# Performance work log

Hardware: AMD Instinct MI355X
Metric: run time of the kernel (lower is better)

## Reference

```python
import jax, jax.numpy as jnp
import numpy as np

N = 100000
E = 1600000
DIMS = [64, 64, 64, 32]  # input -> hidden -> hidden -> num_classes
NEG_SLOPE = 0.01  # F.leaky_relu default


def setup_inputs() -> dict:
    key = jax.random.key(0)
    ks = jax.random.split(key, 8)
    inp = {
        "x": jax.random.normal(ks[0], (N, DIMS[0]), dtype=jnp.float32),
        "edge_index": jax.random.randint(ks[1], (2, E), 0, N, dtype=jnp.int64),
    }
    # GCNConv linear weights (glorot-ish scale) and biases
    for i in range(3):
        d_in, d_out = DIMS[i], DIMS[i + 1]
        scale = (2.0 / (d_in + d_out)) ** 0.5
        inp[f"W{i+1}"] = jax.random.normal(ks[2 + i], (d_in, d_out), dtype=jnp.float32) * scale
        inp[f"b{i+1}"] = jnp.zeros((d_out,), dtype=jnp.float32)
    return inp


def _gcn_conv(x, src, dst, norm, W, b):
    # x' = D^-1/2 (A+I) D^-1/2 (x W) + b
    h = x @ W                                   # [N, d_out]
    msg = h[src] * norm[:, None]                # gather + edge scaling  [E+N, d_out]
    out = jax.ops.segment_sum(msg, dst, num_segments=N)  # scatter-add
    return out + b


def reference(x, edge_index, W1, b1, W2, b2, W3, b3):
    loops = jnp.arange(N, dtype=edge_index.dtype)
    src = jnp.concatenate([edge_index[0], loops])  # add self-loops
    dst = jnp.concatenate([edge_index[1], loops])
    deg = jax.ops.segment_sum(jnp.ones_like(src, dtype=x.dtype), dst, num_segments=N)
    deg_isqrt = jax.lax.rsqrt(deg)              # deg >= 1 due to self-loops
    norm = deg_isqrt[src] * deg_isqrt[dst]      # [E+N]

    embeddings = []
    h = x
    for i, (W, b) in enumerate([(W1, b1), (W2, b2), (W3, b3)]):
        h = _gcn_conv(h, src, dst, norm, W, b)
        if i < 2:
            h = jnp.where(h >= 0, h, NEG_SLOPE * h)  # leaky_relu
        embeddings.append(h)
    return tuple(embeddings)
```

## Files before the change

kernel.cpp:

```cpp
#include <hip/hip_runtime.h>
#include <hip/hip_bf16.h>

typedef __hip_bfloat16 bf16;
typedef __attribute__((ext_vector_type(8))) short bf16x8;
typedef __attribute__((ext_vector_type(4))) short bf16x4;
typedef __attribute__((ext_vector_type(4))) float f32x4;

constexpr int BLK = 256;
constexpr int SCAN2_T = 512;
constexpr int NBLK = 400;

__device__ inline float s2f(short s) {
    union { unsigned u; float f; } z;
    z.u = ((unsigned)(unsigned short)s) << 16;
    return z.f;
}
__device__ inline short f2s(float f) {
    union { bf16 h; short s; } u;
    u.h = __float2bfloat16(f);
    return u.s;
}

__global__ void bucket_hist(const int* __restrict__ dst, int* __restrict__ blockhist,
                            int E, int EPB, int NB) {
    __shared__ int h[512];
    for (int i = threadIdx.x; i < NB; i += BLK) h[i] = 0;
    __syncthreads();
    int lo = blockIdx.x * EPB;
    int hi = min(E, lo + EPB);
    for (int t = lo + threadIdx.x; t < hi; t += BLK)
        atomicAdd(&h[dst[t] >> 8], 1);
    __syncthreads();
    for (int i = threadIdx.x; i < NB; i += BLK)
        blockhist[i * NBLK + blockIdx.x] = h[i];
}

__global__ void colscan_kernel(int* __restrict__ blockhist, int* __restrict__ btotal) {
    __shared__ int s[SCAN2_T];
    int b = blockIdx.x;
    int t = threadIdx.x;
    int v = (t < NBLK) ? blockhist[b * NBLK + t] : 0;
    s[t] = v;
    __syncthreads();
    for (int off = 1; off < SCAN2_T; off <<= 1) {
        int add = (t >= off) ? s[t - off] : 0;
        __syncthreads();
        s[t] += add;
        __syncthreads();
    }
    if (t < NBLK) blockhist[b * NBLK + t] = s[t] - v;
    if (t == SCAN2_T - 1) btotal[b] = s[SCAN2_T - 1];
}

__global__ void scan2_kernel(int* __restrict__ bsum, int nb) {
    __shared__ int s[SCAN2_T];
    int t = threadIdx.x;
    int v = (t < nb) ? bsum[t] : 0;
    s[t] = v;
    __syncthreads();
    for (int off = 1; off < SCAN2_T; off <<= 1) {
        int add = (t >= off) ? s[t - off] : 0;
        __syncthreads();
        s[t] += add;
        __syncthreads();
    }
    if (t < nb) bsum[t] = s[t] - v;
}

__global__ void bucket_scatter(const int* __restrict__ src, const int* __restrict__ dst,
                               const int* __restrict__ blockhist, const int* __restrict__ bbase,
                               int2* __restrict__ ssd, int E, int EPB, int NB) {
    __shared__ int h[512];
    for (int i = threadIdx.x; i < NB; i += BLK)
        h[i] = bbase[i] + blockhist[i * NBLK + blockIdx.x];
    __syncthreads();
    int lo = blockIdx.x * EPB;
    int hi = min(E, lo + EPB);
    for (int t = lo + threadIdx.x; t < hi; t += BLK) {
        int d = dst[t];
        int pos = atomicAdd(&h[d >> 8], 1);
        int2 e; e.x = src[t]; e.y = d;
        ssd[pos] = e;
    }
}

__global__ void bucket_csr(const int2* __restrict__ ssd, const int* __restrict__ bbase,
                           int* __restrict__ col, int* __restrict__ deg,
                           int* __restrict__ row_ptr, float* __restrict__ dinv,
                           int N, int E, int NB) {
    __shared__ int dloc[256];
    __shared__ int ss[256];
    __shared__ int cur[256];
    int b = blockIdx.x;
    int t = threadIdx.x;
    int lo = bbase[b];
    int hi = (b + 1 < NB) ? bbase[b + 1] : E;
    dloc[t] = 0;
    __syncthreads();
    for (int j = lo + t; j < hi; j += BLK)
        atomicAdd(&dloc[ssd[j].y & 255], 1);
    __syncthreads();
    int own = dloc[t];
    ss[t] = own;
    __syncthreads();
    for (int off = 1; off < 256; off <<= 1) {
        int add = (t >= off) ? ss[t - off] : 0;
        __syncthreads();
        ss[t] += add;
        __syncthreads();
    }
    int excl = ss[t] - own;
    cur[t] = lo + excl;
    int node = (b << 8) + t;
    if (node < N) {
        deg[node] = own;
        row_ptr[node] = lo + excl;
        dinv[node] = rsqrtf((float)own + 1.0f);
    }
    __syncthreads();
    for (int j = lo + t; j < hi; j += BLK) {
        int2 e = ssd[j];
        int p = atomicAdd(&cur[e.y & 255], 1);
        col[p] = e.x;
    }
}

__global__ void wconv_all(const float* __restrict__ W1, const float* __restrict__ W2,
                          const float* __restrict__ W3, bf16* __restrict__ WT1,
                          bf16* __restrict__ WT2, bf16* __restrict__ WT3) {
    int idx = blockIdx.x * blockDim.x + threadIdx.x;
    if (idx < 4096) {
        int k = idx >> 6, c = idx & 63;
        WT1[c * 64 + k] = __float2bfloat16(W1[idx]);
    } else if (idx < 8192) {
        int i = idx - 4096, k = i >> 6, c = i & 63;
        WT2[c * 64 + k] = __float2bfloat16(W2[i]);
    } else if (idx < 10240) {
        int i = idx - 8192, k = i >> 5, c = i & 31;
        WT3[c * 64 + k] = __float2bfloat16(W3[i]);
    }
}

template <int DOUT, bool AF32>
__global__ void mfma_gemm(const void* __restrict__ inv, const bf16* __restrict__ WT,
                          const float* __restrict__ dinv, bf16* __restrict__ hlin, int n) {
    constexpr int NT = DOUT / 16;
    const int lane = threadIdx.x & 63;
    const int wave = threadIdx.x >> 6;
    const int q = lane >> 4;
    const int l16 = lane & 15;
    const int row0 = blockIdx.x * 64 + wave * 16;

    int arow = row0 + l16;
    if (arow >= n) arow = n - 1;

    bf16x8 a0, a1;
    if (AF32) {
        const float* in = (const float*)inv;
        const float* p = in + (size_t)arow * 64 + q * 8;
        float4 f0 = *(const float4*)(p);
        float4 f1 = *(const float4*)(p + 4);
        float4 g0 = *(const float4*)(p + 32);
        float4 g1 = *(const float4*)(p + 36);
        bf16 t0[8] = {__float2bfloat16(f0.x), __float2bfloat16(f0.y), __float2bfloat16(f0.z), __float2bfloat16(f0.w),
                      __float2bfloat16(f1.x), __float2bfloat16(f1.y), __float2bfloat16(f1.z), __float2bfloat16(f1.w)};
        bf16 t1[8] = {__float2bfloat16(g0.x), __float2bfloat16(g0.y), __float2bfloat16(g0.z), __float2bfloat16(g0.w),
                      __float2bfloat16(g1.x), __float2bfloat16(g1.y), __float2bfloat16(g1.z), __float2bfloat16(g1.w)};
        __builtin_memcpy(&a0, t0, 16);
        __builtin_memcpy(&a1, t1, 16);
    } else {
        const bf16* in = (const bf16*)inv;
        a0 = *(const bf16x8*)(in + (size_t)arow * 64 + q * 8);
        a1 = *(const bf16x8*)(in + (size_t)arow * 64 + 32 + q * 8);
    }

    f32x4 acc[NT];
#pragma unroll
    for (int ct = 0; ct < NT; ++ct) {
        const bf16* wrow = WT + (size_t)(ct * 16 + l16) * 64 + q * 8;
        bf16x8 b0 = *(const bf16x8*)(wrow);
        bf16x8 b1 = *(const bf16x8*)(wrow + 32);
        f32x4 c = {0.f, 0.f, 0.f, 0.f};
        c = __builtin_amdgcn_mfma_f32_16x16x32_bf16(a0, b0, c, 0, 0, 0);
        c = __builtin_amdgcn_mfma_f32_16x16x32_bf16(a1, b1, c, 0, 0, 0);
        acc[ct] = c;
    }

    float dv[4];
#pragma unroll
    for (int r = 0; r < 4; ++r) {
        int rr = row0 + q * 4 + r;
        dv[r] = (rr < n) ? dinv[rr] : 0.0f;
    }
#pragma unroll
    for (int ct = 0; ct < NT; ++ct) {
#pragma unroll
        for (int r = 0; r < 4; ++r) {
            int rr = row0 + q * 4 + r;
            if (rr < n)
                hlin[(size_t)rr * DOUT + ct * 16 + l16] = __float2bfloat16(acc[ct][r] * dv[r]);
        }
    }
}

template <bool LEAKY>
__global__ void agg64_kernel(const int* __restrict__ row_ptr, const int* __restrict__ deg,
                             const int* __restrict__ col, const bf16* __restrict__ hlin,
                             const float* __restrict__ dinv, const float* __restrict__ b,
                             float* __restrict__ out, bf16* __restrict__ actb, int n) {
    int node = (blockIdx.x * blockDim.x + threadIdx.x) >> 6;
    int lane = threadIdx.x & 63;
    if (node >= n) return;
    const int g = lane >> 3;
    const int fl = lane & 7;

    float acc[8] = {0.f, 0.f, 0.f, 0.f, 0.f, 0.f, 0.f, 0.f};
    if (g == 0) {
        bf16x8 sv = *(const bf16x8*)(hlin + (size_t)node * 64 + (fl << 3));
#pragma unroll
        for (int k = 0; k < 8; ++k) acc[k] = s2f(sv[k]);
    }

    const int beg = row_ptr[node];
    const int end = beg + deg[node];
    int j = beg;
    for (; j + 16 <= end; j += 16) {
        int c0 = col[j + g];
        int c1 = col[j + 8 + g];
        bf16x8 v0 = *(const bf16x8*)(hlin + (size_t)c0 * 64 + (fl << 3));
        bf16x8 v1 = *(const bf16x8*)(hlin + (size_t)c1 * 64 + (fl << 3));
#pragma unroll
        for (int k = 0; k < 8; ++k) acc[k] += s2f(v0[k]) + s2f(v1[k]);
    }
    if (j + 8 <= end) {
        int c = col[j + g];
        bf16x8 v = *(const bf16x8*)(hlin + (size_t)c * 64 + (fl << 3));
#pragma unroll
        for (int k = 0; k < 8; ++k) acc[k] += s2f(v[k]);
        j += 8;
    }
    if (j + g < end) {
        int c = col[j + g];
        bf16x8 v = *(const bf16x8*)(hlin + (size_t)c * 64 + (fl << 3));
#pragma unroll
        for (int k = 0; k < 8; ++k) acc[k] += s2f(v[k]);
    }

#pragma unroll
    for (int k = 0; k < 8; ++k) acc[k] += __shfl_xor(acc[k], 8);
#pragma unroll
    for (int k = 0; k < 8; ++k) acc[k] += __shfl_xor(acc[k], 16);
#pragma unroll
    for (int k = 0; k < 8; ++k) acc[k] += __shfl_xor(acc[k], 32);

    const float dv = dinv[node];
    const float4 bb0 = *(const float4*)(b + (fl << 3));
    const float4 bb1 = *(const float4*)(b + (fl << 3) + 4);
    float vals[8];
    vals[0] = acc[0] * dv + bb0.x;
    vals[1] = acc[1] * dv + bb0.y;
    vals[2] = acc[2] * dv + bb0.z;
    vals[3] = acc[3] * dv + bb0.w;
    vals[4] = acc[4] * dv + bb1.x;
    vals[5] = acc[5] * dv + bb1.y;
    vals[6] = acc[6] * dv + bb1.z;
    vals[7] = acc[7] * dv + bb1.w;
    if (LEAKY) {
#pragma unroll
        for (int k = 0; k < 8; ++k) vals[k] = (vals[k] >= 0.0f) ? vals[k] : 0.01f * vals[k];
    }
    if (g == 0) {
        float* op = out + (size_t)node * 64 + (fl << 3);
        f32x4 o0 = {vals[0], vals[1], vals[2], vals[3]};
        f32x4 o1 = {vals[4], vals[5], vals[6], vals[7]};
        __builtin_nontemporal_store(o0, (f32x4*)op);
        __builtin_nontemporal_store(o1, (f32x4*)(op + 4));
        if (actb) {
            bf16x8 ob;
#pragma unroll
            for (int k = 0; k < 8; ++k) ob[k] = f2s(vals[k]);
            *(bf16x8*)(actb + (size_t)node * 64 + (fl << 3)) = ob;
        }
    }
}

__global__ void agg32_kernel(const int* __restrict__ row_ptr, const int* __restrict__ deg,
                             const int* __restrict__ col, const bf16* __restrict__ hlin,
                             const float* __restrict__ dinv, const float* __restrict__ b,
                             float* __restrict__ out, int n) {
    int node = (blockIdx.x * blockDim.x + threadIdx.x) >> 6;
    int lane = threadIdx.x & 63;
    if (node >= n) return;
    const int g = lane >> 3;
    const int fl = lane & 7;

    float acc[4] = {0.f, 0.f, 0.f, 0.f};
    if (g == 0) {
        bf16x4 sv = *(const bf16x4*)(hlin + (size_t)node * 32 + (fl << 2));
#pragma unroll
        for (int k = 0; k < 4; ++k) acc[k] = s2f(sv[k]);
    }

    const int beg = row_ptr[node];
    const int end = beg + deg[node];
    int j = beg;
    for (; j + 16 <= end; j += 16) {
        int c0 = col[j + g];
        int c1 = col[j + 8 + g];
        bf16x4 v0 = *(const bf16x4*)(hlin + (size_t)c0 * 32 + (fl << 2));
        bf16x4 v1 = *(const bf16x4*)(hlin + (size_t)c1 * 32 + (fl << 2));
#pragma unroll
        for (int k = 0; k < 4; ++k) acc[k] += s2f(v0[k]) + s2f(v1[k]);
    }
    if (j + 8 <= end) {
        int c = col[j + g];
        bf16x4 v = *(const bf16x4*)(hlin + (size_t)c * 32 + (fl << 2));
#pragma unroll
        for (int k = 0; k < 4; ++k) acc[k] += s2f(v[k]);
        j += 8;
    }
    if (j + g < end) {
        int c = col[j + g];
        bf16x4 v = *(const bf16x4*)(hlin + (size_t)c * 32 + (fl << 2));
#pragma unroll
        for (int k = 0; k < 4; ++k) acc[k] += s2f(v[k]);
    }

#pragma unroll
    for (int k = 0; k < 4; ++k) acc[k] += __shfl_xor(acc[k], 8);
#pragma unroll
    for (int k = 0; k < 4; ++k) acc[k] += __shfl_xor(acc[k], 16);
#pragma unroll
    for (int k = 0; k < 4; ++k) acc[k] += __shfl_xor(acc[k], 32);

    const float dv = dinv[node];
    const float4 bb = *(const float4*)(b + (fl << 2));
    float vals[4];
    vals[0] = acc[0] * dv + bb.x;
    vals[1] = acc[1] * dv + bb.y;
    vals[2] = acc[2] * dv + bb.z;
    vals[3] = acc[3] * dv + bb.w;
    if (g == 0) {
        f32x4 o = {vals[0], vals[1], vals[2], vals[3]};
        __builtin_nontemporal_store(o, (f32x4*)(out + (size_t)node * 32 + (fl << 2)));
    }
}

extern "C" void kernel_launch(void* const* d_in, const int* in_sizes, int n_in,
                              void* d_out, int out_size, void* d_ws, size_t ws_size,
                              hipStream_t stream) {
    const float* x  = (const float*)d_in[0];
    const int*   ei = (const int*)d_in[1];
    const float* W1 = (const float*)d_in[2];
    const float* b1 = (const float*)d_in[3];
    const float* W2 = (const float*)d_in[4];
    const float* b2 = (const float*)d_in[5];
    const float* W3 = (const float*)d_in[6];
    const float* b3 = (const float*)d_in[7];
    float* out = (float*)d_out;

    const int N = in_sizes[0] / 64;
    const int E = in_sizes[1] / 2;
    const int* src = ei;
    const int* dst = ei + E;

    const int NB  = (N + 255) >> 8;
    const int EPB = (E + NBLK - 1) / NBLK;

    char* w = (char*)d_ws;
    auto take = [&](size_t bytes) { char* p = w; w += (bytes + 15) & ~(size_t)15; return p; };
    int*   col       = (int*)take((size_t)E * 4);
    int2*  ssd       = (int2*)take((size_t)E * 8);
    bf16*  hlin      = (bf16*)take((size_t)N * 64 * 2);
    bf16*  actb      = (bf16*)take((size_t)N * 64 * 2);
    bf16*  WT1       = (bf16*)take(64 * 64 * 2);
    bf16*  WT2       = (bf16*)take(64 * 64 * 2);
    bf16*  WT3       = (bf16*)take(32 * 64 * 2);
    int*   deg       = (int*)take((size_t)N * 4);
    int*   row_ptr   = (int*)take((size_t)N * 4);
    float* dinv      = (float*)take((size_t)N * 4);
    int*   blockhist = (int*)take((size_t)NB * NBLK * 4);
    int*   btotal    = (int*)take((size_t)SCAN2_T * 4);

    float* out0 = out;
    float* out1 = out + (size_t)N * 64;
    float* out2 = out + (size_t)N * 128;

    const int gemmBlocks = (N + 63) / 64;

    bucket_hist<<<NBLK, BLK, 0, stream>>>(dst, blockhist, E, EPB, NB);
    colscan_kernel<<<NB, SCAN2_T, 0, stream>>>(blockhist, btotal);
    scan2_kernel<<<1, SCAN2_T, 0, stream>>>(btotal, NB);
    bucket_scatter<<<NBLK, BLK, 0, stream>>>(src, dst, blockhist, btotal, ssd, E, EPB, NB);
    bucket_csr<<<NB, BLK, 0, stream>>>(ssd, btotal, col, deg, row_ptr, dinv, N, E, NB);

    wconv_all<<<40, BLK, 0, stream>>>(W1, W2, W3, WT1, WT2, WT3);

    mfma_gemm<64, true><<<gemmBlocks, BLK, 0, stream>>>(x, WT1, dinv, hlin, N);
    agg64_kernel<true><<<((size_t)N * 64 + BLK - 1) / BLK, BLK, 0, stream>>>(
        row_ptr, deg, col, hlin, dinv, b1, out0, actb, N);

    mfma_gemm<64, false><<<gemmBlocks, BLK, 0, stream>>>(actb, WT2, dinv, hlin, N);
    agg64_kernel<true><<<((size_t)N * 64 + BLK - 1) / BLK, BLK, 0, stream>>>(
        row_ptr, deg, col, hlin, dinv, b2, out1, actb, N);

    mfma_gemm<32, false><<<gemmBlocks, BLK, 0, stream>>>(actb, WT3, dinv, hlin, N);
    agg32_kernel<<<((size_t)N * 64 + BLK - 1) / BLK, BLK, 0, stream>>>(
        row_ptr, deg, col, hlin, dinv, b3, out2, N);
}
```

Measured before the change: 314.9 us.

## Pack four nodes per wavefront in aggregation kernels with padded zero row

Aggregation kernels now assign four nodes to each 64-lane wavefront, 16 lanes per node, with two neighbor slots instead of eight. The neighbor loop runs a uniform trip count (max degree among the four nodes), sends out-of-range lanes to a zeroed pad row in hlin, and prefetches the next column index. This cuts the wasted lanes that occur when a node with about 16 neighbors is spread over eight slots, and it removes two shuffle-reduction stages. The cost is a longer serial chain per node and divergence padding toward the largest degree in each group. For agg32 the pad index 2*n points at the same zeroed row under 32-wide addressing, which relies on the extra padded allocation.

```diff
diff --git a/kernel.cpp b/kernel.cpp
--- a/kernel.cpp
+++ b/kernel.cpp
@@ -208,52 +208,48 @@
                              const int* __restrict__ col, const bf16* __restrict__ hlin,
                              const float* __restrict__ dinv, const float* __restrict__ b,
                              float* __restrict__ out, bf16* __restrict__ actb, int n) {
-    int node = (blockIdx.x * blockDim.x + threadIdx.x) >> 6;
-    int lane = threadIdx.x & 63;
-    if (node >= n) return;
-    const int g = lane >> 3;
+    const int wid = (blockIdx.x * blockDim.x + threadIdx.x) >> 6;
+    const int lane = threadIdx.x & 63;
+    const int sub = lane >> 4;
+    const int g = (lane >> 3) & 1;
     const int fl = lane & 7;
-
-    float acc[8] = {0.f, 0.f, 0.f, 0.f, 0.f, 0.f, 0.f, 0.f};
-    if (g == 0) {
-        bf16x8 sv = *(const bf16x8*)(hlin + (size_t)node * 64 + (fl << 3));
+    const int node = wid * 4 + sub;
+    const int PAD = n;
+
+    const bool valid = node < n;
+    const int nc = valid ? node : n - 1;
+    const int beg = row_ptr[nc];
+    const int dg = valid ? deg[nc] : 0;
+    const int end = beg + dg;
+
+    float acc[8];
+    {
+        int c0 = (valid && g == 0) ? node : PAD;
+        bf16x8 sv = *(const bf16x8*)(hlin + (size_t)c0 * 64 + (fl << 3));
 #pragma unroll
         for (int k = 0; k < 8; ++k) acc[k] = s2f(sv[k]);
     }
 
-    const int beg = row_ptr[node];
-    const int end = beg + deg[node];
-    int j = beg;
-    for (; j + 16 <= end; j += 16) {
-        int c0 = col[j + g];
-        int c1 = col[j + 8 + g];
-        bf16x8 v0 = *(const bf16x8*)(hlin + (size_t)c0 * 64 + (fl << 3));
-        bf16x8 v1 = *(const bf16x8*)(hlin + (size_t)c1 * 64 + (fl << 3));
-#pragma unroll
-        for (int k = 0; k < 8; ++k) acc[k] += s2f(v0[k]) + s2f(v1[k]);
-    }
-    if (j + 8 <= end) {
-        int c = col[j + g];
+    int m = dg;
+    m = max(m, __shfl_xor(m, 16));
+    m = max(m, __shfl_xor(m, 32));
+    const int iters = (m + 1) >> 1;
+
+    int idx = beg + g;
+    int cv = col[idx < end ? idx : 0];
+    for (int j = 0; j < iters; ++j) {
+        const int c = (idx < end) ? cv : PAD;
+        idx += 2;
+        cv = col[idx < end ? idx : 0];
         bf16x8 v = *(const bf16x8*)(hlin + (size_t)c * 64 + (fl << 3));
 #pragma unroll
         for (int k = 0; k < 8; ++k) acc[k] += s2f(v[k]);
-        j += 8;
-    }
-    if (j + g < end) {
-        int c = col[j + g];
-        bf16x8 v = *(const bf16x8*)(hlin + (size_t)c * 64 + (fl << 3));
-#pragma unroll
-        for (int k = 0; k < 8; ++k) acc[k] += s2f(v[k]);
     }
 
 #pragma unroll
     for (int k = 0; k < 8; ++k) acc[k] += __shfl_xor(acc[k], 8);
-#pragma unroll
-    for (int k = 0; k < 8; ++k) acc[k] += __shfl_xor(acc[k], 16);
-#pragma unroll
-    for (int k = 0; k < 8; ++k) acc[k] += __shfl_xor(acc[k], 32);
-
-    const float dv = dinv[node];
+
+    const float dv = dinv[nc];
     const float4 bb0 = *(const float4*)(b + (fl << 3));
     const float4 bb1 = *(const float4*)(b + (fl << 3) + 4);
     float vals[8];
@@ -269,7 +265,7 @@
 #pragma unroll
         for (int k = 0; k < 8; ++k) vals[k] = (vals[k] >= 0.0f) ? vals[k] : 0.01f * vals[k];
     }
-    if (g == 0) {
+    if (valid && g == 0) {
         float* op = out + (size_t)node * 64 + (fl << 3);
         f32x4 o0 = {vals[0], vals[1], vals[2], vals[3]};
         f32x4 o1 = {vals[4], vals[5], vals[6], vals[7]};
@@ -288,59 +284,55 @@
                              const int* __restrict__ col, const bf16* __restrict__ hlin,
                              const float* __restrict__ dinv, const float* __restrict__ b,
                              float* __restrict__ out, int n) {
-    int node = (blockIdx.x * blockDim.x + threadIdx.x) >> 6;
-    int lane = threadIdx.x & 63;
-    if (node >= n) return;
-    const int g = lane >> 3;
+    const int wid = (blockIdx.x * blockDim.x + threadIdx.x) >> 6;
+    const int lane = threadIdx.x & 63;
+    const int sub = lane >> 4;
+    const int g = (lane >> 3) & 1;
     const int fl = lane & 7;
-
-    float acc[4] = {0.f, 0.f, 0.f, 0.f};
-    if (g == 0) {
-        bf16x4 sv = *(const bf16x4*)(hlin + (size_t)node * 32 + (fl << 2));
+    const int node = wid * 4 + sub;
+    const int PAD = 2 * n;
+
+    const bool valid = node < n;
+    const int nc = valid ? node : n - 1;
+    const int beg = row_ptr[nc];
+    const int dg = valid ? deg[nc] : 0;
+    const int end = beg + dg;
+
+    float acc[4];
+    {
+        int c0 = (valid && g == 0) ? node : PAD;
+        bf16x4 sv = *(const bf16x4*)(hlin + (size_t)c0 * 32 + (fl << 2));
 #pragma unroll
         for (int k = 0; k < 4; ++k) acc[k] = s2f(sv[k]);
     }
 
-    const int beg = row_ptr[node];
-    const int end = beg + deg[node];
-    int j = beg;
-    for (; j + 16 <= end; j += 16) {
-        int c0 = col[j + g];
-        int c1 = col[j + 8 + g];
-        bf16x4 v0 = *(const bf16x4*)(hlin + (size_t)c0 * 32 + (fl << 2));
-        bf16x4 v1 = *(const bf16x4*)(hlin + (size_t)c1 * 32 + (fl << 2));
-#pragma unroll
-        for (int k = 0; k < 4; ++k) acc[k] += s2f(v0[k]) + s2f(v1[k]);
-    }
-    if (j + 8 <= end) {
-        int c = col[j + g];
+    int m = dg;
+    m = max(m, __shfl_xor(m, 16));
+    m = max(m, __shfl_xor(m, 32));
+    const int iters = (m + 1) >> 1;
+
+    int idx = beg + g;
+    int cv = col[idx < end ? idx : 0];
+    for (int j = 0; j < iters; ++j) {
+        const int c = (idx < end) ? cv : PAD;
+        idx += 2;
+        cv = col[idx < end ? idx : 0];
         bf16x4 v = *(const bf16x4*)(hlin + (size_t)c * 32 + (fl << 2));
 #pragma unroll
         for (int k = 0; k < 4; ++k) acc[k] += s2f(v[k]);
-        j += 8;
-    }
-    if (j + g < end) {
-        int c = col[j + g];
-        bf16x4 v = *(const bf16x4*)(hlin + (size_t)c * 32 + (fl << 2));
-#pragma unroll
-        for (int k = 0; k < 4; ++k) acc[k] += s2f(v[k]);
     }
 
 #pragma unroll
     for (int k = 0; k < 4; ++k) acc[k] += __shfl_xor(acc[k], 8);
-#pragma unroll
-    for (int k = 0; k < 4; ++k) acc[k] += __shfl_xor(acc[k], 16);
-#pragma unroll
-    for (int k = 0; k < 4; ++k) acc[k] += __shfl_xor(acc[k], 32);
-
-    const float dv = dinv[node];
+
+    const float dv = dinv[nc];
     const float4 bb = *(const float4*)(b + (fl << 2));
     float vals[4];
     vals[0] = acc[0] * dv + bb.x;
     vals[1] = acc[1] * dv + bb.y;
     vals[2] = acc[2] * dv + bb.z;
     vals[3] = acc[3] * dv + bb.w;
-    if (g == 0) {
+    if (valid && g == 0) {
         f32x4 o = {vals[0], vals[1], vals[2], vals[3]};
         __builtin_nontemporal_store(o, (f32x4*)(out + (size_t)node * 32 + (fl << 2)));
     }
@@ -371,7 +363,7 @@
     auto take = [&](size_t bytes) { char* p = w; w += (bytes + 15) & ~(size_t)15; return p; };
     int*   col       = (int*)take((size_t)E * 4);
     int2*  ssd       = (int2*)take((size_t)E * 8);
-    bf16*  hlin      = (bf16*)take((size_t)N * 64 * 2);
+    bf16*  hlin      = (bf16*)take(((size_t)N * 64 + 64) * 2);
     bf16*  actb      = (bf16*)take((size_t)N * 64 * 2);
     bf16*  WT1       = (bf16*)take(64 * 64 * 2);
     bf16*  WT2       = (bf16*)take(64 * 64 * 2);
@@ -387,6 +379,10 @@
     float* out2 = out + (size_t)N * 128;
 
     const int gemmBlocks = (N + 63) / 64;
+    const int aggWaves = (N + 3) / 4;
+    const int aggBlocks = (aggWaves * 64 + BLK - 1) / BLK;
+
+    hipMemsetAsync(hlin + (size_t)N * 64, 0, 128, stream);
 
     bucket_hist<<<NBLK, BLK, 0, stream>>>(dst, blockhist, E, EPB, NB);
     colscan_kernel<<<NB, SCAN2_T, 0, stream>>>(blockhist, btotal);
@@ -397,14 +393,14 @@
     wconv_all<<<40, BLK, 0, stream>>>(W1, W2, W3, WT1, WT2, WT3);
 
     mfma_gemm<64, true><<<gemmBlocks, BLK, 0, stream>>>(x, WT1, dinv, hlin, N);
-    agg64_kernel<true><<<((size_t)N * 64 + BLK - 1) / BLK, BLK, 0, stream>>>(
+    agg64_kernel<true><<<aggBlocks, BLK, 0, stream>>>(
         row_ptr, deg, col, hlin, dinv, b1, out0, actb, N);
 
     mfma_gemm<64, false><<<gemmBlocks, BLK, 0, stream>>>(actb, WT2, dinv, hlin, N);
-    agg64_kernel<true><<<((size_t)N * 64 + BLK - 1) / BLK, BLK, 0, stream>>>(
+    agg64_kernel<true><<<aggBlocks, BLK, 0, stream>>>(
         row_ptr, deg, col, hlin, dinv, b2, out1, actb, N);
 
     mfma_gemm<32, false><<<gemmBlocks, BLK, 0, stream>>>(actb, WT3, dinv, hlin, N);
-    agg32_kernel<<<((size_t)N * 64 + BLK - 1) / BLK, BLK, 0, stream>>>(
+    agg32_kernel<<<aggBlocks, BLK, 0, stream>>>(
         row_ptr, deg, col, hlin, dinv, b3, out2, N);
 }
```

Result: faster. 295.6 us (-6.1%).
